# Kernel tuning notes

Measured on AMD Instinct MI355X. Metric: run time of the kernel, lower is better.

The kernel has to match this reference:

```python
import jax, jax.numpy as jnp
import numpy as np

N = 50000       # nodes
E = 800000      # edges (before self loops)
F_IN = 128      # in_channels
HID = 128       # hidden_channels
HEADS = 4
NEG_SLOPE = 0.2  # PyG GATConv default leaky_relu slope


def gat_conv(x, src, dst, W, a_src, a_dst, b, heads, out_ch, concat):
    """PyG-style GATConv (eval mode, dropout off).
    x: [N,F_in]; src/dst: [E'] edge endpoints (edge j->i means src=j, dst=i);
    W: [F_in, heads*out_ch]; a_src,a_dst: [heads,out_ch]; b: [out dim].
    """
    n = x.shape[0]
    h = (x @ W).reshape(n, heads, out_ch)              # [N,H,C]
    alpha_src = jnp.sum(h * a_src, axis=-1)            # [N,H]
    alpha_dst = jnp.sum(h * a_dst, axis=-1)            # [N,H]
    e = jax.nn.leaky_relu(alpha_src[src] + alpha_dst[dst], NEG_SLOPE)  # [E',H]
    # segment softmax over incoming edges of each destination node
    m = jax.ops.segment_max(e, dst, num_segments=n)    # [N,H]
    ex = jnp.exp(e - m[dst])
    den = jax.ops.segment_sum(ex, dst, num_segments=n)
    alpha = ex / den[dst]                              # [E',H]
    out = jax.ops.segment_sum(h[src] * alpha[:, :, None], dst, num_segments=n)  # [N,H,C]
    out = out.reshape(n, heads * out_ch) if concat else out.mean(axis=1)
    return out + b


def setup_inputs() -> dict:
    key = jax.random.key(0)
    ks = jax.random.split(key, 10)
    s = 0.1
    return {
        "x": jax.random.normal(ks[0], (N, F_IN), jnp.float32),
        "edge_index": jax.random.randint(ks[1], (2, E), 0, N),
        # layer 1: heads=4, out_ch=HID//HEADS=32, concat
        "W1": jax.random.normal(ks[2], (F_IN, HID), jnp.float32) * s,
        "att_src1": jax.random.normal(ks[3], (HEADS, HID // HEADS), jnp.float32) * s,
        "att_dst1": jax.random.normal(ks[4], (HEADS, HID // HEADS), jnp.float32) * s,
        "b1": jnp.zeros((HID,), jnp.float32),
        # layer 2: heads=1, out_ch=HID, mean (concat=False)
        "W2": jax.random.normal(ks[5], (HID, HID), jnp.float32) * s,
        "att_src2": jax.random.normal(ks[6], (1, HID), jnp.float32) * s,
        "att_dst2": jax.random.normal(ks[7], (1, HID), jnp.float32) * s,
        "b2": jnp.zeros((HID,), jnp.float32),
    }


def reference(x, edge_index, W1, att_src1, att_dst1, b1, W2, att_src2, att_dst2, b2):
    n = x.shape[0]
    loops = jnp.arange(n, dtype=edge_index.dtype)      # add_self_loops=True (PyG default)
    src = jnp.concatenate([edge_index[0], loops])
    dst = jnp.concatenate([edge_index[1], loops])
    h = gat_conv(x, src, dst, W1, att_src1, att_dst1, b1, HEADS, HID // HEADS, True)
    h = jax.nn.elu(h)                                  # ELU between layers; dropout is identity in eval
    out = gat_conv(h, src, dst, W2, att_src2, att_dst2, b2, 1, HID, False)
    return out
```

## Files before the change

kernel.cpp:

```cpp
#include <hip/hip_runtime.h>
#include <math.h>

typedef unsigned short u16;
typedef unsigned int u32;
typedef __attribute__((ext_vector_type(8))) short short8v;
typedef __attribute__((ext_vector_type(4))) float float4v;

#define BKT_SH 7
#define BKT_CAP 4096
#define BKT_MAX 512
#define TILE 8192

__device__ __forceinline__ u16 f2bf(float f) {
    u32 u = __float_as_uint(f);
    u = (u + 0x7FFFu + ((u >> 16) & 1u)) >> 16;
    return (u16)u;
}
__device__ __forceinline__ float bflo(u32 u) { return __uint_as_float(u << 16); }
__device__ __forceinline__ float bfhi(u32 u) { return __uint_as_float(u & 0xFFFF0000u); }

__global__ void prep_w(const float* __restrict__ W1, const float* __restrict__ W2,
                       u16* __restrict__ WT1, u16* __restrict__ WT2) {
    int t = blockIdx.x * 256 + threadIdx.x;
    int which = t >> 14, idx = t & 16383;
    int k = idx >> 7, c = idx & 127;
    const float* W = which ? W2 : W1;
    u16* WT = which ? WT2 : WT1;
    WT[c * 128 + k] = f2bf(W[k * 128 + c]);
}

template <int INBF16, int H>
__global__ __launch_bounds__(256) void gemm_mfma(const void* __restrict__ Xv,
                                                 const u16* __restrict__ WT,
                                                 const float* __restrict__ a_src,
                                                 const float* __restrict__ a_dst,
                                                 u16* __restrict__ Hb,
                                                 float* __restrict__ AS,
                                                 float* __restrict__ AD, int n) {
    __shared__ __align__(16) u16 xs[64][136];
    __shared__ __align__(16) u16 ws[128][136];
    const int t = threadIdx.x;
    const int n0 = blockIdx.x * 64;

    {
        const uint4* src = (const uint4*)WT;
        #pragma unroll
        for (int i = 0; i < 8; ++i) {
            int idx = t + i * 256;
            int row = idx >> 4, oct = idx & 15;
            uint4 v = src[idx];
            *(uint4*)&ws[row][oct * 8] = v;
        }
    }
    if (INBF16) {
        const u16* X = (const u16*)Xv;
        #pragma unroll
        for (int i = 0; i < 4; ++i) {
            int idx = t + i * 256;
            int row = idx >> 4, oct = idx & 15;
            uint4 v = make_uint4(0, 0, 0, 0);
            if (n0 + row < n) v = *(const uint4*)&X[(size_t)(n0 + row) * 128 + oct * 8];
            *(uint4*)&xs[row][oct * 8] = v;
        }
    } else {
        const float* X = (const float*)Xv;
        #pragma unroll
        for (int i = 0; i < 8; ++i) {
            int idx = t + i * 256;
            int row = idx >> 5, quad = idx & 31;
            float4 v = make_float4(0.f, 0.f, 0.f, 0.f);
            if (n0 + row < n) v = *(const float4*)&X[(size_t)(n0 + row) * 128 + quad * 4];
            u32 lo = (u32)f2bf(v.x) | ((u32)f2bf(v.y) << 16);
            u32 hi = (u32)f2bf(v.z) | ((u32)f2bf(v.w) << 16);
            *(uint2*)&xs[row][quad * 4] = make_uint2(lo, hi);
        }
    }
    __syncthreads();

    const int wave = t >> 6, lane = t & 63;
    const int r0 = wave * 16;
    const int kcol = lane & 15;
    const int arow = r0 + kcol;
    const int kb = (lane >> 4) * 8;

    float4v acc[8];
    #pragma unroll
    for (int j = 0; j < 8; ++j) acc[j] = (float4v){0.f, 0.f, 0.f, 0.f};

    #pragma unroll
    for (int kk = 0; kk < 4; ++kk) {
        const int k0 = kk * 32 + kb;
        short8v a = *(const short8v*)&xs[arow][k0];
        #pragma unroll
        for (int j = 0; j < 8; ++j) {
            short8v b = *(const short8v*)&ws[j * 16 + kcol][k0];
            acc[j] = __builtin_amdgcn_mfma_f32_16x16x32_bf16(a, b, acc[j], 0, 0, 0);
        }
    }

    const int rbase = n0 + r0 + (lane >> 4) * 4;
    #pragma unroll
    for (int j = 0; j < 8; ++j) {
        #pragma unroll
        for (int r = 0; r < 4; ++r) {
            int row = rbase + r;
            if (row < n) Hb[(size_t)row * 128 + j * 16 + kcol] = f2bf(acc[j][r]);
        }
    }

    float av[8], bv[8];
    #pragma unroll
    for (int j = 0; j < 8; ++j) {
        av[j] = a_src[j * 16 + kcol];
        bv[j] = a_dst[j * 16 + kcol];
    }

    if (H == 4) {
        float ps[4][4], pd[4][4];
        #pragma unroll
        for (int r = 0; r < 4; ++r)
            #pragma unroll
            for (int h = 0; h < 4; ++h) {
                ps[r][h] = acc[2*h][r] * av[2*h] + acc[2*h+1][r] * av[2*h+1];
                pd[r][h] = acc[2*h][r] * bv[2*h] + acc[2*h+1][r] * bv[2*h+1];
            }
        #pragma unroll
        for (int o = 8; o >= 1; o >>= 1)
            #pragma unroll
            for (int r = 0; r < 4; ++r)
                #pragma unroll
                for (int h = 0; h < 4; ++h) {
                    ps[r][h] += __shfl_xor(ps[r][h], o);
                    pd[r][h] += __shfl_xor(pd[r][h], o);
                }
        float wvs = 0.f, wvd = 0.f;
        #pragma unroll
        for (int r = 0; r < 4; ++r)
            #pragma unroll
            for (int h = 0; h < 4; ++h)
                if (kcol == r * 4 + h) { wvs = ps[r][h]; wvd = pd[r][h]; }
        int node = rbase + (kcol >> 2);
        if (node < n) {
            AS[node * 4 + (kcol & 3)] = wvs;
            AD[node * 4 + (kcol & 3)] = wvd;
        }
    } else {
        float ps[4], pd[4];
        #pragma unroll
        for (int r = 0; r < 4; ++r) {
            float s_ = 0.f, d_ = 0.f;
            #pragma unroll
            for (int j = 0; j < 8; ++j) {
                s_ += acc[j][r] * av[j];
                d_ += acc[j][r] * bv[j];
            }
            ps[r] = s_; pd[r] = d_;
        }
        #pragma unroll
        for (int o = 8; o >= 1; o >>= 1)
            #pragma unroll
            for (int r = 0; r < 4; ++r) {
                ps[r] += __shfl_xor(ps[r], o);
                pd[r] += __shfl_xor(pd[r], o);
            }
        float val = 0.f;
        #pragma unroll
        for (int r = 0; r < 4; ++r)
            if ((kcol & 3) == r) val = (kcol < 4) ? ps[r] : pd[r];
        int node = rbase + (kcol & 3);
        if (kcol < 8 && node < n) {
            if (kcol < 4) AS[node] = val;
            else          AD[node] = val;
        }
    }
}

__global__ __launch_bounds__(256) void bucket_append(
    const int* __restrict__ ei, int* __restrict__ bcnt,
    u32* __restrict__ bkt, int E, int etot, int nbkt) {
    __shared__ u32 ent[TILE];
    __shared__ int hist[BKT_MAX], lstart[BKT_MAX], gbase[BKT_MAX], cur[BKT_MAX];
    __shared__ int sc[BKT_MAX];
    const int t = threadIdx.x;
    const int e0 = blockIdx.x * TILE;
    const int cnt = min(TILE, etot - e0);

    for (int i = t; i < BKT_MAX; i += 256) { hist[i] = 0; }
    __syncthreads();

    for (int i = t; i < cnt; i += 256) {
        int e = e0 + i;
        int d = (e < E) ? ei[E + e] : e - E;
        atomicAdd(&hist[d >> BKT_SH], 1);
    }
    __syncthreads();

    sc[t] = hist[t];
    sc[t + 256] = hist[t + 256];
    __syncthreads();
    for (int off = 1; off < BKT_MAX; off <<= 1) {
        int i0 = t, i1 = t + 256;
        int v0 = (i0 >= off) ? sc[i0 - off] : 0;
        int v1 = (i1 >= off) ? sc[i1 - off] : 0;
        __syncthreads();
        sc[i0] += v0;
        sc[i1] += v1;
        __syncthreads();
    }
    for (int i = t; i < BKT_MAX; i += 256) {
        int ls = sc[i] - hist[i];
        lstart[i] = ls;
        cur[i] = ls;
        gbase[i] = (i < nbkt && hist[i] > 0) ? atomicAdd(&bcnt[i * 16], hist[i]) : 0;
    }
    __syncthreads();

    for (int i = t; i < cnt; i += 256) {
        int e = e0 + i;
        int s, d;
        if (e < E) { s = ei[e]; d = ei[E + e]; } else { s = d = e - E; }
        int p = atomicAdd(&cur[d >> BKT_SH], 1);
        ent[p] = ((u32)d << 16) | (u32)s;
    }
    __syncthreads();

    for (int i = t; i < cnt; i += 256) {
        u32 en = ent[i];
        int b = en >> (16 + BKT_SH);
        int pos = gbase[b] + (i - lstart[b]);
        if (pos < BKT_CAP) bkt[(size_t)b * BKT_CAP + pos] = en;
    }
}

__global__ void bscan(const int* __restrict__ bcnt, int* __restrict__ bbase,
                      int nbkt, int* __restrict__ offsets, int n, int etot) {
    __shared__ int tmp[BKT_MAX];
    int t = threadIdx.x;
    int v = (t < nbkt) ? min(bcnt[t * 16], BKT_CAP) : 0;
    tmp[t] = v;
    __syncthreads();
    for (int off = 1; off < BKT_MAX; off <<= 1) {
        int u = (t >= off) ? tmp[t - off] : 0;
        __syncthreads();
        tmp[t] += u;
        __syncthreads();
    }
    if (t < nbkt) bbase[t] = tmp[t] - v;
    if (t == 0) offsets[n] = etot;
}

__global__ __launch_bounds__(256) void bucket_csr(
    const u32* __restrict__ bkt, const int* __restrict__ bcnt,
    const int* __restrict__ bbase, int* __restrict__ offsets,
    int* __restrict__ csr_src, int n) {
    __shared__ u32 ent[BKT_CAP];
    __shared__ int hist[128], pr[128], cur[128];
    const int b = blockIdx.x;
    const int t = threadIdx.x;
    const int cnt = min(bcnt[b * 16], BKT_CAP);
    const int base = bbase[b];

    for (int i = t; i < cnt; i += 256) ent[i] = bkt[(size_t)b * BKT_CAP + i];
    if (t < 128) hist[t] = 0;
    __syncthreads();
    for (int i = t; i < cnt; i += 256) atomicAdd(&hist[(ent[i] >> 16) & 127], 1);
    __syncthreads();
    if (t < 128) pr[t] = hist[t];
    __syncthreads();
    #pragma unroll
    for (int off = 1; off < 128; off <<= 1) {
        int u = (t >= off && t < 128) ? pr[t - off] : 0;
        __syncthreads();
        if (t < 128) pr[t] += u;
        __syncthreads();
    }
    if (t < 128) {
        int excl = pr[t] - hist[t];
        int d = b * 128 + t;
        if (d < n) offsets[d] = base + excl;
        cur[t] = excl;
    }
    __syncthreads();
    for (int i = t; i < cnt; i += 256) {
        u32 en = ent[i];
        int dl = (en >> 16) & 127;
        int pos = base + atomicAdd(&cur[dl], 1);
        csr_src[pos] = (int)(en & 0xFFFFu);
    }
}

template <int H, int MODE>
__global__ __launch_bounds__(256) void node_fused(
    const int* __restrict__ offsets, const int* __restrict__ csr_src,
    const float* __restrict__ AS, const float* __restrict__ AD,
    const u16* __restrict__ Hb, const float* __restrict__ bias,
    void* __restrict__ OUT, int n) {
    const int wid = threadIdx.x >> 6, lane = threadIdx.x & 63;
    const int d = blockIdx.x * 4 + wid;
    if (d >= n) return;
    const int off = offsets[d];
    const int deg = offsets[d + 1] - off;

    constexpr int SCH = (H == 4) ? 16 : 64;
    const int slot = (H == 4) ? (lane & 15) : lane;
    const int g    = (H == 4) ? (lane >> 4) : 0;
    const float adv = AD[d * H + g];

    const int which = lane >> 5;
    const int cq    = lane & 31;
    const int ghead = (H == 4) ? (cq >> 3) : 0;

    float acc0 = 0.f, acc1 = 0.f, acc2 = 0.f, acc3 = 0.f;
    float smp = 0.f;

    bool v = slot < deg;
    int   s_cur = v ? csr_src[off + slot] : 0;
    float x_cur = v ? AS[s_cur * H + g] : 0.f;
    float vm_cur = v ? 1.f : 0.f;

    for (int k0 = 0; k0 < deg; k0 += SCH) {
        int kn = k0 + SCH + slot;
        bool vn = kn < deg;
        int   s_nxt = vn ? csr_src[off + kn] : 0;
        float x_nxt = vn ? AS[s_nxt * H + g] : 0.f;

        float e = x_cur + adv;
        float lr = e > 0.f ? e : 0.2f * e;
        float a_l = vm_cur * __expf(lr);
        smp += a_l;

        const int rem = min(SCH, deg - k0);
        const int npairs = (rem + 1) >> 1;
        #pragma unroll
        for (int p = 0; p < SCH / 2; ++p) {
            if (p >= npairs) break;
            int eslot = p * 2 + which;
            int aidx = (H == 4) ? (ghead * 16 + eslot) : eslot;
            float al = __shfl(a_l, aidx);
            int   sj = __shfl(s_cur, aidx);
            uint2 u2 = *(const uint2*)&Hb[(size_t)sj * 128 + cq * 4];
            acc0 += al * bflo(u2.x);
            acc1 += al * bfhi(u2.x);
            acc2 += al * bflo(u2.y);
            acc3 += al * bfhi(u2.y);
        }
        s_cur = s_nxt; x_cur = x_nxt; vm_cur = vn ? 1.f : 0.f;
    }

    #pragma unroll
    for (int o = (H == 4 ? 8 : 32); o >= 1; o >>= 1)
        smp += __shfl_xor(smp, o);
    float den = (H == 4) ? __shfl(smp, ghead * 16) : smp;
    const float dinv = 1.f / den;

    acc0 += __shfl_xor(acc0, 32);
    acc1 += __shfl_xor(acc1, 32);
    acc2 += __shfl_xor(acc2, 32);
    acc3 += __shfl_xor(acc3, 32);

    if (lane < 32) {
        const float4 bv = *(const float4*)&bias[cq * 4];
        float o0 = acc0 * dinv + bv.x;
        float o1 = acc1 * dinv + bv.y;
        float o2 = acc2 * dinv + bv.z;
        float o3 = acc3 * dinv + bv.w;
        if (MODE == 0) {
            o0 = o0 > 0.f ? o0 : expm1f(o0);
            o1 = o1 > 0.f ? o1 : expm1f(o1);
            o2 = o2 > 0.f ? o2 : expm1f(o2);
            o3 = o3 > 0.f ? o3 : expm1f(o3);
            uint2 pk;
            pk.x = (u32)f2bf(o0) | ((u32)f2bf(o1) << 16);
            pk.y = (u32)f2bf(o2) | ((u32)f2bf(o3) << 16);
            *(uint2*)&((u16*)OUT)[(size_t)d * 128 + cq * 4] = pk;
        } else {
            float* O = (float*)OUT;
            *(float4*)&O[(size_t)d * 128 + cq * 4] = make_float4(o0, o1, o2, o3);
        }
    }
}

extern "C" void kernel_launch(void* const* d_in, const int* in_sizes, int n_in,
                              void* d_out, int out_size, void* d_ws, size_t ws_size,
                              hipStream_t stream) {
    const float* x   = (const float*)d_in[0];
    const int*   ei  = (const int*)d_in[1];
    const float* W1  = (const float*)d_in[2];
    const float* as1 = (const float*)d_in[3];
    const float* ad1 = (const float*)d_in[4];
    const float* b1  = (const float*)d_in[5];
    const float* W2  = (const float*)d_in[6];
    const float* as2 = (const float*)d_in[7];
    const float* ad2 = (const float*)d_in[8];
    const float* b2  = (const float*)d_in[9];
    float* out = (float*)d_out;

    const int n = in_sizes[0] / 128;
    const int E = in_sizes[1] / 2;
    const int etot = E + n;
    const int nbkt = (n + 127) >> BKT_SH;

    char* p = (char*)d_ws;
    u16* Hb1 = (u16*)p; p += (size_t)n * 128 * 2;
    u16* Xb2 = (u16*)p; p += (size_t)n * 128 * 2;
    u16* Hb2 = (u16*)p; p += (size_t)n * 128 * 2;
    float* AS = (float*)p; p += (size_t)n * 4 * 4;
    float* AD = (float*)p; p += (size_t)n * 4 * 4;
    u16* WT1 = (u16*)p; p += 32768;
    u16* WT2 = (u16*)p; p += 32768;
    u32* bkt     = (u32*)p; p += (size_t)BKT_MAX * BKT_CAP * 4;
    int* bcnt    = (int*)p; p += (size_t)BKT_MAX * 16 * 4;
    int* bbase   = (int*)p; p += (size_t)BKT_MAX * 4;
    int* csr_src = (int*)p; p += (size_t)etot * 4;
    int* offsets = (int*)p; p += (size_t)(n + 1) * 4;

    const int ggrid = (n + 63) / 64;
    const int ngrid = (n + 3) / 4;
    const int agrid = (etot + TILE - 1) / TILE;

    prep_w<<<128, 256, 0, stream>>>(W1, W2, WT1, WT2);
    (void)hipMemsetAsync(bcnt, 0, (size_t)BKT_MAX * 16 * 4, stream);
    bucket_append<<<agrid, 256, 0, stream>>>(ei, bcnt, bkt, E, etot, nbkt);
    bscan<<<1, BKT_MAX, 0, stream>>>(bcnt, bbase, nbkt, offsets, n, etot);
    bucket_csr<<<nbkt, 256, 0, stream>>>(bkt, bcnt, bbase, offsets, csr_src, n);

    gemm_mfma<0, 4><<<ggrid, 256, 0, stream>>>(x, WT1, as1, ad1, Hb1, AS, AD, n);
    node_fused<4, 0><<<ngrid, 256, 0, stream>>>(offsets, csr_src, AS, AD, Hb1, b1, Xb2, n);

    gemm_mfma<1, 1><<<ggrid, 256, 0, stream>>>(Xb2, WT2, as2, ad2, Hb2, AS, AD, n);
    node_fused<1, 1><<<ngrid, 256, 0, stream>>>(offsets, csr_src, AS, AD, Hb2, b2, out, n);
}
```

Baseline: 170.6 us.

## Fuse bucket scan into bucket_csr and simplify per-edge aggregation loop

Removes the separate single-block bscan launch. Each bucket_csr block now redundantly computes the prefix sum over bucket counts in shared memory. Separately, node_fused drops the chunked shuffle-broadcast scheme: each half-wave now processes edges directly, two at a time, loading csr_src and AS per lane and computing the exp weight itself before reducing across halves. This removes a kernel launch and the shuffles, but adds redundant index/score loads and exp work per lane, and loses the one-chunk prefetch.

```diff
diff --git a/kernel.cpp b/kernel.cpp
--- a/kernel.cpp
+++ b/kernel.cpp
@@ -232,33 +232,31 @@
     }
 }
 
-__global__ void bscan(const int* __restrict__ bcnt, int* __restrict__ bbase,
-                      int nbkt, int* __restrict__ offsets, int n, int etot) {
-    __shared__ int tmp[BKT_MAX];
-    int t = threadIdx.x;
-    int v = (t < nbkt) ? min(bcnt[t * 16], BKT_CAP) : 0;
-    tmp[t] = v;
-    __syncthreads();
-    for (int off = 1; off < BKT_MAX; off <<= 1) {
-        int u = (t >= off) ? tmp[t - off] : 0;
-        __syncthreads();
-        tmp[t] += u;
-        __syncthreads();
-    }
-    if (t < nbkt) bbase[t] = tmp[t] - v;
-    if (t == 0) offsets[n] = etot;
-}
-
 __global__ __launch_bounds__(256) void bucket_csr(
     const u32* __restrict__ bkt, const int* __restrict__ bcnt,
-    const int* __restrict__ bbase, int* __restrict__ offsets,
-    int* __restrict__ csr_src, int n) {
+    int* __restrict__ offsets, int* __restrict__ csr_src,
+    int n, int nbkt, int etot) {
     __shared__ u32 ent[BKT_CAP];
     __shared__ int hist[128], pr[128], cur[128];
+    __shared__ int sc[BKT_MAX];
     const int b = blockIdx.x;
     const int t = threadIdx.x;
+
+    sc[t]       = (t < nbkt)       ? min(bcnt[t * 16], BKT_CAP) : 0;
+    sc[t + 256] = (t + 256 < nbkt) ? min(bcnt[(t + 256) * 16], BKT_CAP) : 0;
+    __syncthreads();
+    for (int off = 1; off < BKT_MAX; off <<= 1) {
+        int i0 = t, i1 = t + 256;
+        int v0 = (i0 >= off) ? sc[i0 - off] : 0;
+        int v1 = (i1 >= off) ? sc[i1 - off] : 0;
+        __syncthreads();
+        sc[i0] += v0;
+        sc[i1] += v1;
+        __syncthreads();
+    }
     const int cnt = min(bcnt[b * 16], BKT_CAP);
-    const int base = bbase[b];
+    const int base = sc[b] - cnt;
+    if (b == 0 && t == 0) offsets[n] = etot;
 
     for (int i = t; i < cnt; i += 256) ent[i] = bkt[(size_t)b * BKT_CAP + i];
     if (t < 128) hist[t] = 0;
@@ -301,69 +299,55 @@
     const int off = offsets[d];
     const int deg = offsets[d + 1] - off;
 
-    constexpr int SCH = (H == 4) ? 16 : 64;
-    const int slot = (H == 4) ? (lane & 15) : lane;
-    const int g    = (H == 4) ? (lane >> 4) : 0;
-    const float adv = AD[d * H + g];
-
     const int which = lane >> 5;
     const int cq    = lane & 31;
     const int ghead = (H == 4) ? (cq >> 3) : 0;
-
-    float acc0 = 0.f, acc1 = 0.f, acc2 = 0.f, acc3 = 0.f;
+    const float adv = AD[d * H + ghead];
+
+    float a0 = 0.f, a1 = 0.f, a2 = 0.f, a3 = 0.f;
     float smp = 0.f;
 
-    bool v = slot < deg;
-    int   s_cur = v ? csr_src[off + slot] : 0;
-    float x_cur = v ? AS[s_cur * H + g] : 0.f;
-    float vm_cur = v ? 1.f : 0.f;
-
-    for (int k0 = 0; k0 < deg; k0 += SCH) {
-        int kn = k0 + SCH + slot;
-        bool vn = kn < deg;
-        int   s_nxt = vn ? csr_src[off + kn] : 0;
-        float x_nxt = vn ? AS[s_nxt * H + g] : 0.f;
-
-        float e = x_cur + adv;
-        float lr = e > 0.f ? e : 0.2f * e;
-        float a_l = vm_cur * __expf(lr);
-        smp += a_l;
-
-        const int rem = min(SCH, deg - k0);
-        const int npairs = (rem + 1) >> 1;
-        #pragma unroll
-        for (int p = 0; p < SCH / 2; ++p) {
-            if (p >= npairs) break;
-            int eslot = p * 2 + which;
-            int aidx = (H == 4) ? (ghead * 16 + eslot) : eslot;
-            float al = __shfl(a_l, aidx);
-            int   sj = __shfl(s_cur, aidx);
-            uint2 u2 = *(const uint2*)&Hb[(size_t)sj * 128 + cq * 4];
-            acc0 += al * bflo(u2.x);
-            acc1 += al * bfhi(u2.x);
-            acc2 += al * bflo(u2.y);
-            acc3 += al * bfhi(u2.y);
-        }
-        s_cur = s_nxt; x_cur = x_nxt; vm_cur = vn ? 1.f : 0.f;
-    }
-
-    #pragma unroll
-    for (int o = (H == 4 ? 8 : 32); o >= 1; o >>= 1)
-        smp += __shfl_xor(smp, o);
-    float den = (H == 4) ? __shfl(smp, ghead * 16) : smp;
-    const float dinv = 1.f / den;
-
-    acc0 += __shfl_xor(acc0, 32);
-    acc1 += __shfl_xor(acc1, 32);
-    acc2 += __shfl_xor(acc2, 32);
-    acc3 += __shfl_xor(acc3, 32);
+    for (int k0 = 0; k0 < deg; k0 += 4) {
+        const int ka = k0 + which;
+        const int kb = k0 + 2 + which;
+        const bool va = ka < deg;
+        const bool vb = kb < deg;
+        const int sa = va ? csr_src[off + ka] : 0;
+        const int sb = vb ? csr_src[off + kb] : 0;
+        const float xa = va ? AS[sa * H + ghead] : 0.f;
+        const float xb = vb ? AS[sb * H + ghead] : 0.f;
+
+        float ea = xa + adv; ea = ea > 0.f ? ea : 0.2f * ea;
+        float eb = xb + adv; eb = eb > 0.f ? eb : 0.2f * eb;
+        const float ala = va ? __expf(ea) : 0.f;
+        const float alb = vb ? __expf(eb) : 0.f;
+        smp += ala + alb;
+
+        if (va) {
+            uint2 u = *(const uint2*)&Hb[(size_t)sa * 128 + cq * 4];
+            a0 += ala * bflo(u.x); a1 += ala * bfhi(u.x);
+            a2 += ala * bflo(u.y); a3 += ala * bfhi(u.y);
+        }
+        if (vb) {
+            uint2 u = *(const uint2*)&Hb[(size_t)sb * 128 + cq * 4];
+            a0 += alb * bflo(u.x); a1 += alb * bfhi(u.x);
+            a2 += alb * bflo(u.y); a3 += alb * bfhi(u.y);
+        }
+    }
+
+    a0  += __shfl_xor(a0, 32);
+    a1  += __shfl_xor(a1, 32);
+    a2  += __shfl_xor(a2, 32);
+    a3  += __shfl_xor(a3, 32);
+    smp += __shfl_xor(smp, 32);
+    const float dinv = 1.f / smp;
 
     if (lane < 32) {
         const float4 bv = *(const float4*)&bias[cq * 4];
-        float o0 = acc0 * dinv + bv.x;
-        float o1 = acc1 * dinv + bv.y;
-        float o2 = acc2 * dinv + bv.z;
-        float o3 = acc3 * dinv + bv.w;
+        float o0 = a0 * dinv + bv.x;
+        float o1 = a1 * dinv + bv.y;
+        float o2 = a2 * dinv + bv.z;
+        float o3 = a3 * dinv + bv.w;
         if (MODE == 0) {
             o0 = o0 > 0.f ? o0 : expm1f(o0);
             o1 = o1 > 0.f ? o1 : expm1f(o1);
@@ -410,7 +394,6 @@
     u16* WT2 = (u16*)p; p += 32768;
     u32* bkt     = (u32*)p; p += (size_t)BKT_MAX * BKT_CAP * 4;
     int* bcnt    = (int*)p; p += (size_t)BKT_MAX * 16 * 4;
-    int* bbase   = (int*)p; p += (size_t)BKT_MAX * 4;
     int* csr_src = (int*)p; p += (size_t)etot * 4;
     int* offsets = (int*)p; p += (size_t)(n + 1) * 4;
 
@@ -421,8 +404,7 @@
     prep_w<<<128, 256, 0, stream>>>(W1, W2, WT1, WT2);
     (void)hipMemsetAsync(bcnt, 0, (size_t)BKT_MAX * 16 * 4, stream);
     bucket_append<<<agrid, 256, 0, stream>>>(ei, bcnt, bkt, E, etot, nbkt);
-    bscan<<<1, BKT_MAX, 0, stream>>>(bcnt, bbase, nbkt, offsets, n, etot);
-    bucket_csr<<<nbkt, 256, 0, stream>>>(bkt, bcnt, bbase, offsets, csr_src, n);
+    bucket_csr<<<nbkt, 256, 0, stream>>>(bkt, bcnt, offsets, csr_src, n, nbkt, etot);
 
     gemm_mfma<0, 4><<<ggrid, 256, 0, stream>>>(x, WT1, as1, ad1, Hb1, AS, AD, n);
     node_fused<4, 0><<<ngrid, 256, 0, stream>>>(offsets, csr_src, AS, AD, Hb1, b1, Xb2, n);
```

Result: slower. 214.0 us (+25.5%).
